# Optimization experiments

Hardware: AMD Instinct MI355X
Metric: run time of the kernel (lower is better)

Reference implementation:

```python
import jax, jax.numpy as jnp
import numpy as np

B, S, DIM, E, K = 8, 8192, 512, 4, 2
EPS = 1e-6


def setup_inputs() -> dict:
    key = jax.random.key(0)
    ks = jax.random.split(key, 4)
    scale = 0.02
    return {
        "x": jax.random.normal(ks[0], (B, S, DIM), dtype=jnp.float32),
        "router_w": jax.random.normal(ks[1], (DIM, E), dtype=jnp.float32) * scale,
        "router_b": jnp.zeros((E,), jnp.float32),
        "expert_w": jax.random.normal(ks[2], (E, DIM, DIM), dtype=jnp.float32) * scale,
        "expert_b": jnp.zeros((E, DIM), jnp.float32),
        "out_w": jax.random.normal(ks[3], (DIM, DIM), dtype=jnp.float32) * scale,
        "out_b": jnp.zeros((DIM,), jnp.float32),
        "norm_w": jnp.ones((DIM,), jnp.float32),
    }


def reference(x, router_w, router_b, expert_w, expert_b, out_w, out_b, norm_w):
    b, s, d = x.shape
    # router
    logits = x @ router_w + router_b                      # [B,S,E]
    topw, topi = jax.lax.top_k(logits, K)                 # [B,S,K]
    topw = jax.nn.softmax(topw, axis=-1)
    t = b * s
    xf = x.reshape(t, d)
    idx = topi.reshape(t, K)
    w = topw.reshape(t, K).astype(x.dtype)
    # dense token-expert weight mask (topk indices are distinct per token)
    mask = jnp.zeros((t, E), x.dtype).at[jnp.arange(t)[:, None], idx].set(w)
    # expert FFN: Linear + SiLU (dropout disabled in eval)
    h = jax.nn.silu(jnp.einsum("td,edh->teh", xf, expert_w) + expert_b)  # [T,E,D]
    comb = jnp.einsum("te,teh->th", mask, h)              # weighted combine
    out = comb @ out_w + out_b
    y = xf + out                                          # residual
    rms = jnp.sqrt(jnp.mean(y * y, axis=-1, keepdims=True) + EPS)
    return (norm_w * (y / rms)).reshape(b, s, d)
```

## Files before the change

kernel.cpp:

```cpp
#include <hip/hip_runtime.h>
#include <hip/hip_bf16.h>
#include <stdint.h>

#define NTOK 65536
#define DIM 512
#define NEXP 4
#define REG 14336

using u16 = unsigned short;
using u32 = unsigned int;
typedef __attribute__((ext_vector_type(4))) float f32x4;
typedef __attribute__((ext_vector_type(8))) short bf16x8;
typedef __attribute__((ext_vector_type(8))) u16 u16x8;
typedef __attribute__((ext_vector_type(4))) u16 u16x4;

__device__ __forceinline__ u16 f2bf(float f) {
  u32 u = __builtin_bit_cast(u32, f);
  u32 r = (u + 0x7FFFu + ((u >> 16) & 1u)) >> 16;
  return (u16)r;
}
__device__ __forceinline__ float bf2f(u16 v) {
  return __builtin_bit_cast(float, (u32)v << 16);
}

#define GLOAD_LDS16(gp, lp)                                                    \
  __builtin_amdgcn_global_load_lds(                                            \
      (const __attribute__((address_space(1))) void*)(gp),                     \
      (__attribute__((address_space(3))) void*)(lp), 16, 0, 0)

#define FENCE asm volatile("" ::: "memory")
#define BARRIER { FENCE; __builtin_amdgcn_s_barrier(); FENCE; }
#define VMCNT_(n) asm volatile("s_waitcnt vmcnt(" #n ")" ::: "memory")
#define VMCNT(n) VMCNT_(n)
#define SB __builtin_amdgcn_sched_barrier(0)

__device__ __forceinline__ const bf16x8* lds_frag(const u16* base, int row, int chunk) {
  return (const bf16x8*)((const char*)base + row * 128 + (((chunk) ^ (row & 7)) << 4));
}

__global__ void packw(const float* __restrict__ ew, const float* __restrict__ ow,
                      u16* __restrict__ ewtp, u16* __restrict__ owt3,
                      int* __restrict__ cnt) {
  if (blockIdx.x == 0 && threadIdx.x < 6) cnt[threadIdx.x] = 0;
  int lane = threadIdx.x & 63, wv = threadIdx.x >> 6;
  int gf = blockIdx.x * 4 + wv;
  int r16 = lane & 15, lg = lane >> 4;
  u16x8 o;
  if (gf < 2048) {
    int hs = gf & 31, T = (gf >> 5) & 15, e = gf >> 9;
    int h = hs * 16 + r16;
    int d0 = T * 32 + lg * 8;
#pragma unroll
    for (int q = 0; q < 8; ++q)
      o[q] = f2bf(ew[((size_t)e * DIM + d0 + q) * DIM + h]);
    *(u16x8*)(ewtp + (size_t)gf * 512 + lane * 8) = o;
  } else {
    int frag = gf - 2048;
    int j = frag & 7, kc = (frag >> 3) & 1, t = (frag >> 4) & 7, strip = frag >> 7;
    int h = strip * 128 + j * 16 + r16;
    int d0 = t * 64 + kc * 32 + lg * 8;
#pragma unroll
    for (int q = 0; q < 8; ++q) o[q] = f2bf(ow[(size_t)(d0 + q) * DIM + h]);
    *(u16x8*)(owt3 + (size_t)frag * 512 + lane * 8) = o;
  }
}

__global__ void router_kernel(const float* __restrict__ x, const float* __restrict__ rw,
                              const float* __restrict__ rb, u16* __restrict__ xb,
                              int* __restrict__ pp, float2* __restrict__ wab) {
  int lane = threadIdx.x & 63, wave = threadIdx.x >> 6;
  size_t t = (size_t)blockIdx.x * 4 + wave;
  const float* xr = x + t * DIM + lane * 8;
  f32x4 v0 = *(const f32x4*)xr;
  f32x4 v1 = *(const f32x4*)(xr + 4);
  float l0 = 0.f, l1 = 0.f, l2 = 0.f, l3 = 0.f;
  const float* rwp = rw + (size_t)lane * 32;
#pragma unroll
  for (int j = 0; j < 8; ++j) {
    float xv = (j < 4) ? v0[j] : v1[j - 4];
    f32x4 r = *(const f32x4*)(rwp + j * 4);
    l0 += xv * r[0]; l1 += xv * r[1]; l2 += xv * r[2]; l3 += xv * r[3];
  }
#pragma unroll
  for (int off = 32; off; off >>= 1) {
    l0 += __shfl_xor(l0, off); l1 += __shfl_xor(l1, off);
    l2 += __shfl_xor(l2, off); l3 += __shfl_xor(l3, off);
  }
  float lv[4] = {l0 + rb[0], l1 + rb[1], l2 + rb[2], l3 + rb[3]};
  int i0 = 0; float b0 = lv[0];
#pragma unroll
  for (int e = 1; e < 4; ++e) if (lv[e] > b0) { b0 = lv[e]; i0 = e; }
  int i1 = (i0 == 0) ? 1 : 0; float b1 = lv[i1];
#pragma unroll
  for (int e = 0; e < 4; ++e) if (e != i0 && lv[e] > b1) { b1 = lv[e]; i1 = e; }
  float ex = __expf(b1 - b0);
  float w0 = 1.0f / (1.0f + ex);
  float w1 = ex * w0;
  if (lane == 0) {
    int a = (i0 < i1) ? i0 : i1;
    int b = (i0 < i1) ? i1 : i0;
    const int ptab[16] = {-1, 0, 1, 2, -1, -1, 3, 4, -1, -1, -1, 5, -1, -1, -1, -1};
    pp[t] = ptab[a * 4 + b];
    float wa = (a == i0) ? w0 : w1;
    float wb = (a == i0) ? w1 : w0;
    wab[t] = make_float2(wa, wb);
  }
  u16x8 o;
#pragma unroll
  for (int j = 0; j < 4; ++j) { o[j] = f2bf(v0[j]); o[4 + j] = f2bf(v1[j]); }
  *(u16x8*)(xb + t * DIM + lane * 8) = o;
}

__global__ void assignscatter(const int* __restrict__ pp, const float2* __restrict__ wab,
                              int* __restrict__ cnt, int* __restrict__ list,
                              float2* __restrict__ wpair) {
  int t = blockIdx.x * 256 + threadIdx.x;
  int lane = threadIdx.x & 63;
  int p = pp[t];
  float2 w = wab[t];
  int pos = 0;
#pragma unroll
  for (int q = 0; q < 6; ++q) {
    unsigned long long m = __ballot(p == q);
    if (p == q) {
      int rank = __popcll(m & ((1ull << lane) - 1ull));
      int leader = __ffsll((long long)m) - 1;
      int base = 0;
      if (lane == leader) base = atomicAdd(&cnt[q], (int)__popcll(m));
      base = __shfl(base, leader);
      pos = base + rank;
    }
  }
  int slot = p * REG + pos;
  if (pos < REG) {
    list[slot] = t;
    wpair[slot] = w;
  }
}

__global__ __launch_bounds__(256, 2) void expert_gemm(
    const u16* __restrict__ xb, const u16* __restrict__ ewtp,
    const float* __restrict__ ebias, const int* __restrict__ cnt,
    const int* __restrict__ list, const float2* __restrict__ wpair,
    u16* __restrict__ comb) {
  __shared__ u16 Asl[3][128 * 64];
  int tid = threadIdx.x, lane = tid & 63, wave = tid >> 6;
  int wy = wave >> 1, wx = wave & 1;
  int b = blockIdx.x;
  int chunk = b >> 5, within = b & 31;
  int panel = chunk * 8 + (within & 7);
  int nblk = within >> 3;
  int p = panel / (REG / 128);
  int m0 = panel * 128;
  int cntp = cnt[p];
  if (m0 - p * REG >= cntp) return;
  int n0 = nblk * 128;
  const int ea2[6] = {0, 0, 0, 1, 1, 2};
  const int eb2[6] = {1, 2, 3, 2, 3, 3};
  int eA = ea2[p], eB = eb2[p];

  int r16 = lane & 15, lg = lane >> 4;
  int rl = lane >> 3;
  int scb = ((lane & 7) ^ rl) * 8;
  int s = r16 & 7;
  int ab0 = (wy * 64 + r16) * 128 + ((s >> 2) << 6) + ((lg ^ (s & 3)) << 4);
  int ab1 = ab0 ^ 64;

  int sid[4];
#pragma unroll
  for (int j = 0; j < 4; ++j) {
    int slot = m0 + wave * 32 + j * 8 + rl;
    int idv = list[slot];
    sid[j] = ((slot - p * REG) < cntp) ? idv : 0;
  }
  const u16* a0b = xb + (size_t)sid[0] * DIM + scb;
  const u16* a1b = xb + (size_t)sid[1] * DIM + scb;
  const u16* a2b = xb + (size_t)sid[2] * DIM + scb;
  const u16* a3b = xb + (size_t)sid[3] * DIM + scb;
  const u16* bpA = ewtp + (size_t)eA * 262144 + (size_t)(n0 / 16 + wx * 4) * 512 + lane * 8;
  const u16* bpB = ewtp + (size_t)eB * 262144 + (size_t)(n0 / 16 + wx * 4) * 512 + lane * 8;

  f32x4 accA[4][4], accB[4][4];
#pragma unroll
  for (int i = 0; i < 4; ++i)
#pragma unroll
    for (int j = 0; j < 4; ++j) { accA[i][j] = (f32x4)(0.f); accB[i][j] = (f32x4)(0.f); }

#define STAGE(BI, KS)                                                          \
  do {                                                                         \
    GLOAD_LDS16(a0b + (KS) * 64, Asl[BI] + (wave * 32) * 64);                  \
    GLOAD_LDS16(a1b + (KS) * 64, Asl[BI] + (wave * 32 + 8) * 64);              \
    GLOAD_LDS16(a2b + (KS) * 64, Asl[BI] + (wave * 32 + 16) * 64);             \
    GLOAD_LDS16(a3b + (KS) * 64, Asl[BI] + (wave * 32 + 24) * 64);             \
  } while (0)
#define LOADB(BV, T32)                                                         \
  do {                                                                         \
    _Pragma("unroll") for (int i = 0; i < 4; ++i) {                            \
      BV[i]     = *(const bf16x8*)(bpA + (T32) * 16384 + i * 512);             \
      BV[4 + i] = *(const bf16x8*)(bpB + (T32) * 16384 + i * 512);             \
    }                                                                          \
  } while (0)

  STAGE(0, 0); SB;
  STAGE(1, 1); SB;
  VMCNT(4);
  BARRIER;

  bf16x8 Bk0[8], Bk1[8];
#define KST(T, WC)                                                             \
  {                                                                            \
    LOADB(Bk0, 2 * (T));                                                       \
    LOADB(Bk1, 2 * (T) + 1);                                                   \
    SB;                                                                        \
    if ((T) + 2 < 8) { STAGE(((T) + 2) % 3, (T) + 2); }                        \
    SB;                                                                        \
    const char* Ab_ = (const char*)Asl[(T) % 3];                               \
    bf16x8 a[4];                                                               \
    _Pragma("unroll") for (int i = 0; i < 4; ++i)                              \
      a[i] = *(const bf16x8*)(Ab_ + ab0 + i * 2048);                           \
    __builtin_amdgcn_s_setprio(1);                                             \
    _Pragma("unroll") for (int i = 0; i < 4; ++i)                              \
      _Pragma("unroll") for (int j = 0; j < 4; ++j)                            \
        accA[i][j] = __builtin_amdgcn_mfma_f32_16x16x32_bf16(a[i], Bk0[j], accA[i][j], 0, 0, 0); \
    _Pragma("unroll") for (int i = 0; i < 4; ++i)                              \
      _Pragma("unroll") for (int j = 0; j < 4; ++j)                            \
        accB[i][j] = __builtin_amdgcn_mfma_f32_16x16x32_bf16(a[i], Bk0[4 + j], accB[i][j], 0, 0, 0); \
    __builtin_amdgcn_s_setprio(0);                                             \
    _Pragma("unroll") for (int i = 0; i < 4; ++i)                              \
      a[i] = *(const bf16x8*)(Ab_ + ab1 + i * 2048);                           \
    __builtin_amdgcn_s_setprio(1);                                             \
    _Pragma("unroll") for (int i = 0; i < 4; ++i)                              \
      _Pragma("unroll") for (int j = 0; j < 4; ++j)                            \
        accA[i][j] = __builtin_amdgcn_mfma_f32_16x16x32_bf16(a[i], Bk1[j], accA[i][j], 0, 0, 0); \
    _Pragma("unroll") for (int i = 0; i < 4; ++i)                              \
      _Pragma("unroll") for (int j = 0; j < 4; ++j)                            \
        accB[i][j] = __builtin_amdgcn_mfma_f32_16x16x32_bf16(a[i], Bk1[4 + j], accB[i][j], 0, 0, 0); \
    __builtin_amdgcn_s_setprio(0);                                             \
    WC;                                                                        \
  }

  KST(0, { VMCNT(4); BARRIER; })
  KST(1, { VMCNT(4); BARRIER; })
  KST(2, { VMCNT(4); BARRIER; })
  KST(3, { VMCNT(4); BARRIER; })
  KST(4, { VMCNT(4); BARRIER; })
  KST(5, { VMCNT(4); BARRIER; })
  KST(6, { VMCNT(0); BARRIER; })
  KST(7, {})
#undef KST
#undef LOADB
#undef STAGE

  float bA4[4], bB4[4];
#pragma unroll
  for (int j = 0; j < 4; ++j) {
    int h = n0 + wx * 64 + j * 16 + r16;
    bA4[j] = ebias[eA * DIM + h];
    bB4[j] = ebias[eB * DIM + h];
  }
#pragma unroll
  for (int i = 0; i < 4; ++i) {
    int rb = wy * 64 + i * 16 + lg * 4;
#pragma unroll
    for (int rr = 0; rr < 4; ++rr) {
      int slot = m0 + rb + rr;
      bool val = (slot - p * REG) < cntp;
      int id = list[slot];
      float2 wv = wpair[slot];
#pragma unroll
      for (int j = 0; j < 4; ++j) {
        float zA = accA[i][j][rr] + bA4[j];
        float zB = accB[i][j][rr] + bB4[j];
        float sA = zA / (1.0f + __expf(-zA));
        float sB = zB / (1.0f + __expf(-zB));
        float v = wv.x * sA + wv.y * sB;
        if (val) {
          int h = n0 + wx * 64 + j * 16 + r16;
          comb[(size_t)id * DIM + h] = f2bf(v);
        }
      }
    }
  }
}

__global__ __launch_bounds__(256, 2) void outnorm(
    const u16* __restrict__ comb, const u16* __restrict__ owt3,
    const float* __restrict__ ob, const u16* __restrict__ xb,
    const float* __restrict__ nw, float* __restrict__ out) {
  __shared__ u16 As[3][64 * 64];
  __shared__ float rowsum[64][4];
  int tid = threadIdx.x, lane = tid & 63, w = tid >> 6;
  int m0 = blockIdx.x * 64;
  int r16 = lane & 15, lg = lane >> 4;
  int rl = lane >> 3;
  int scb = ((lane & 7) ^ rl) * 8;
  int n0w = w * 128;

  f32x4 acc[8][4];
#pragma unroll
  for (int j = 0; j < 8; ++j)
#pragma unroll
    for (int i = 0; i < 4; ++i) acc[j][i] = (f32x4)(0.f);

#define OSTG(bi, ks)                                                           \
  _Pragma("unroll") for (int jj = 0; jj < 2; ++jj) {                           \
    GLOAD_LDS16(comb + (size_t)(m0 + w * 16 + jj * 8 + rl) * DIM + (ks) * 64 + scb, \
                As[bi] + (w * 16 + jj * 8) * 64);                              \
  }
#define LOADB(BV, HH)                                                          \
  {                                                                            \
    const u16* bp_ = owt3 +                                                    \
        ((size_t)(((w * 8 + ((HH) >> 1)) * 2 + ((HH) & 1)) * 8)) * 512 + lane * 8; \
    _Pragma("unroll") for (int jj = 0; jj < 8; ++jj)                           \
      BV[jj] = *(const bf16x8*)(bp_ + jj * 512);                               \
  }
#define HSTEP(H, BC, BN, WC)                                                   \
  {                                                                            \
    if (((H) & 1) == 0 && ((H) >> 1) + 2 < 8) OSTG((((H) >> 1) + 2) % 3, ((H) >> 1) + 2); \
    if ((H) + 1 < 16) LOADB(BN, (H) + 1);                                      \
    bf16x8 af[4];                                                              \
    _Pragma("unroll") for (int ii = 0; ii < 4; ++ii)                           \
      af[ii] = *lds_frag(As[((H) >> 1) % 3], ii * 16 + r16, ((H) & 1) * 4 + lg); \
    __builtin_amdgcn_s_setprio(1);                                             \
    _Pragma("unroll") for (int jj = 0; jj < 8; ++jj)                           \
      _Pragma("unroll") for (int ii = 0; ii < 4; ++ii)                         \
        acc[jj][ii] = __builtin_amdgcn_mfma_f32_16x16x32_bf16(BC[jj], af[ii], acc[jj][ii], 0, 0, 0); \
    __builtin_amdgcn_s_setprio(0);                                             \
    WC;                                                                        \
  }

  bf16x8 BE[8], BO[8];
  OSTG(0, 0); OSTG(1, 1);
  LOADB(BE, 0);
  VMCNT(10);
  BARRIER;

  HSTEP(0,  BE, BO, {})
  HSTEP(1,  BO, BE, { VMCNT(10); BARRIER; })
  HSTEP(2,  BE, BO, {})
  HSTEP(3,  BO, BE, { VMCNT(10); BARRIER; })
  HSTEP(4,  BE, BO, {})
  HSTEP(5,  BO, BE, { VMCNT(10); BARRIER; })
  HSTEP(6,  BE, BO, {})
  HSTEP(7,  BO, BE, { VMCNT(10); BARRIER; })
  HSTEP(8,  BE, BO, {})
  HSTEP(9,  BO, BE, { VMCNT(10); BARRIER; })
  HSTEP(10, BE, BO, {})
  HSTEP(11, BO, BE, { VMCNT(10); BARRIER; })
  HSTEP(12, BE, BO, {})
  HSTEP(13, BO, BE, { VMCNT(8); BARRIER; })
  HSTEP(14, BE, BO, {})
  HSTEP(15, BO, BE, {})
#undef HSTEP
#undef LOADB
#undef OSTG

  float part[4] = {0.f, 0.f, 0.f, 0.f};
#pragma unroll
  for (int hj = 0; hj < 8; ++hj) {
    int h0 = n0w + hj * 16 + lg * 4;
    f32x4 obv = *(const f32x4*)(ob + h0);
#pragma unroll
    for (int ti = 0; ti < 4; ++ti) {
      int t = m0 + ti * 16 + r16;
      u16x4 xv4 = *(const u16x4*)(xb + (size_t)t * DIM + h0);
#pragma unroll
      for (int rr = 0; rr < 4; ++rr) {
        float yv = bf2f(xv4[rr]) + acc[hj][ti][rr] + obv[rr];
        acc[hj][ti][rr] = yv;
        part[ti] += yv * yv;
      }
    }
  }
#pragma unroll
  for (int ti = 0; ti < 4; ++ti) {
    part[ti] += __shfl_xor(part[ti], 16);
    part[ti] += __shfl_xor(part[ti], 32);
  }
  if (lane < 16) {
#pragma unroll
    for (int ti = 0; ti < 4; ++ti) rowsum[ti * 16 + r16][w] = part[ti];
  }
  __syncthreads();
  float inv[4];
#pragma unroll
  for (int ti = 0; ti < 4; ++ti) {
    int tr = ti * 16 + r16;
    float s = rowsum[tr][0] + rowsum[tr][1] + rowsum[tr][2] + rowsum[tr][3];
    inv[ti] = 1.0f / sqrtf(s * (1.0f / 512.0f) + 1e-6f);
  }
#pragma unroll
  for (int hj = 0; hj < 8; ++hj) {
    int h0 = n0w + hj * 16 + lg * 4;
    f32x4 nwv = *(const f32x4*)(nw + h0);
#pragma unroll
    for (int ti = 0; ti < 4; ++ti) {
      int t = m0 + ti * 16 + r16;
      f32x4 o;
#pragma unroll
      for (int rr = 0; rr < 4; ++rr) o[rr] = acc[hj][ti][rr] * inv[ti] * nwv[rr];
      *(f32x4*)(out + (size_t)t * DIM + h0) = o;
    }
  }
}

extern "C" void kernel_launch(void* const* d_in, const int* in_sizes, int n_in,
                              void* d_out, int out_size, void* d_ws, size_t ws_size,
                              hipStream_t stream) {
  const float* x  = (const float*)d_in[0];
  const float* rw = (const float*)d_in[1];
  const float* rb = (const float*)d_in[2];
  const float* ew = (const float*)d_in[3];
  const float* eb = (const float*)d_in[4];
  const float* ow = (const float*)d_in[5];
  const float* ob = (const float*)d_in[6];
  const float* nw = (const float*)d_in[7];
  float* out = (float*)d_out;

  char* ws = (char*)d_ws;
  u16*   xb    = (u16*)(ws);
  u16*   combb = (u16*)(ws + 67108864);
  int*   pp    = (int*)(ws + 67108864);
  float2* wab  = (float2*)(ws + 67108864 + 262144);
  u16*   ewtp  = (u16*)(ws + 134217728);
  u16*   owt3  = (u16*)(ws + 136314880);
  int*   list  = (int*)(ws + 136839168);
  float2* wpair = (float2*)(ws + 136839168 + 344064);
  int*   cnt   = (int*)(ws + 136839168 + 344064 + 688128);

  packw<<<640, 256, 0, stream>>>(ew, ow, ewtp, owt3, cnt);
  router_kernel<<<NTOK / 4, 256, 0, stream>>>(x, rw, rb, xb, pp, wab);
  assignscatter<<<NTOK / 256, 256, 0, stream>>>(pp, wab, cnt, list, wpair);
  expert_gemm<<<dim3(6 * REG / 128 * 4), 256, 0, stream>>>(xb, ewtp, eb, cnt, list, wpair, combb);
  outnorm<<<dim3(NTOK / 64), 256, 0, stream>>>(combb, owt3, ob, xb, nw, out);
}
```

Baseline: 317.7 us.

## Halve outnorm row tile to 32 and drop B-fragment double buffering

The outnorm kernel now processes 32 token rows per block instead of 64, halving accumulators and LDS, and raises the launch-bounds occupancy hint to 3 blocks per CU. The register double-buffered prefetch of the output weight fragments is removed; weights are now loaded inside each step, and the vmcnt waits are adjusted to match. This trades more weight reloads per token and less latency hiding for higher occupancy and twice as many blocks.

Measured after the change: 322.5 us. About the same (+1.5%).

```diff
diff --git a/kernel.cpp b/kernel.cpp
--- a/kernel.cpp
+++ b/kernel.cpp
@@ -283,85 +283,80 @@
   }
 }
 
-__global__ __launch_bounds__(256, 2) void outnorm(
+__global__ __launch_bounds__(256, 3) void outnorm(
     const u16* __restrict__ comb, const u16* __restrict__ owt3,
     const float* __restrict__ ob, const u16* __restrict__ xb,
     const float* __restrict__ nw, float* __restrict__ out) {
-  __shared__ u16 As[3][64 * 64];
-  __shared__ float rowsum[64][4];
+  __shared__ u16 As[3][32 * 64];
+  __shared__ float rowsum[32][4];
   int tid = threadIdx.x, lane = tid & 63, w = tid >> 6;
-  int m0 = blockIdx.x * 64;
+  int m0 = blockIdx.x * 32;
   int r16 = lane & 15, lg = lane >> 4;
   int rl = lane >> 3;
   int scb = ((lane & 7) ^ rl) * 8;
   int n0w = w * 128;
 
-  f32x4 acc[8][4];
+  f32x4 acc[8][2];
 #pragma unroll
   for (int j = 0; j < 8; ++j)
 #pragma unroll
-    for (int i = 0; i < 4; ++i) acc[j][i] = (f32x4)(0.f);
+    for (int i = 0; i < 2; ++i) acc[j][i] = (f32x4)(0.f);
 
 #define OSTG(bi, ks)                                                           \
-  _Pragma("unroll") for (int jj = 0; jj < 2; ++jj) {                           \
-    GLOAD_LDS16(comb + (size_t)(m0 + w * 16 + jj * 8 + rl) * DIM + (ks) * 64 + scb, \
-                As[bi] + (w * 16 + jj * 8) * 64);                              \
-  }
-#define LOADB(BV, HH)                                                          \
-  {                                                                            \
-    const u16* bp_ = owt3 +                                                    \
-        ((size_t)(((w * 8 + ((HH) >> 1)) * 2 + ((HH) & 1)) * 8)) * 512 + lane * 8; \
-    _Pragma("unroll") for (int jj = 0; jj < 8; ++jj)                           \
-      BV[jj] = *(const bf16x8*)(bp_ + jj * 512);                               \
-  }
-#define HSTEP(H, BC, BN, WC)                                                   \
+  GLOAD_LDS16(comb + (size_t)(m0 + w * 8 + rl) * DIM + (ks) * 64 + scb,        \
+              As[bi] + (w * 8) * 64)
+
+#define HSTEP(H, WC)                                                           \
   {                                                                            \
     if (((H) & 1) == 0 && ((H) >> 1) + 2 < 8) OSTG((((H) >> 1) + 2) % 3, ((H) >> 1) + 2); \
-    if ((H) + 1 < 16) LOADB(BN, (H) + 1);                                      \
-    bf16x8 af[4];                                                              \
-    _Pragma("unroll") for (int ii = 0; ii < 4; ++ii)                           \
+    bf16x8 bw[8];                                                              \
+    {                                                                          \
+      const u16* bp_ = owt3 +                                                  \
+          ((size_t)(((w * 8 + ((H) >> 1)) * 2 + ((H) & 1)) * 8)) * 512 + lane * 8; \
+      _Pragma("unroll") for (int jj = 0; jj < 8; ++jj)                         \
+        bw[jj] = *(const bf16x8*)(bp_ + jj * 512);                             \
+    }                                                                          \
+    bf16x8 af[2];                                                              \
+    _Pragma("unroll") for (int ii = 0; ii < 2; ++ii)                           \
       af[ii] = *lds_frag(As[((H) >> 1) % 3], ii * 16 + r16, ((H) & 1) * 4 + lg); \
     __builtin_amdgcn_s_setprio(1);                                             \
     _Pragma("unroll") for (int jj = 0; jj < 8; ++jj)                           \
-      _Pragma("unroll") for (int ii = 0; ii < 4; ++ii)                         \
-        acc[jj][ii] = __builtin_amdgcn_mfma_f32_16x16x32_bf16(BC[jj], af[ii], acc[jj][ii], 0, 0, 0); \
+      _Pragma("unroll") for (int ii = 0; ii < 2; ++ii)                         \
+        acc[jj][ii] = __builtin_amdgcn_mfma_f32_16x16x32_bf16(bw[jj], af[ii], acc[jj][ii], 0, 0, 0); \
     __builtin_amdgcn_s_setprio(0);                                             \
     WC;                                                                        \
   }
 
-  bf16x8 BE[8], BO[8];
   OSTG(0, 0); OSTG(1, 1);
-  LOADB(BE, 0);
-  VMCNT(10);
+  VMCNT(1);
   BARRIER;
 
-  HSTEP(0,  BE, BO, {})
-  HSTEP(1,  BO, BE, { VMCNT(10); BARRIER; })
-  HSTEP(2,  BE, BO, {})
-  HSTEP(3,  BO, BE, { VMCNT(10); BARRIER; })
-  HSTEP(4,  BE, BO, {})
-  HSTEP(5,  BO, BE, { VMCNT(10); BARRIER; })
-  HSTEP(6,  BE, BO, {})
-  HSTEP(7,  BO, BE, { VMCNT(10); BARRIER; })
-  HSTEP(8,  BE, BO, {})
-  HSTEP(9,  BO, BE, { VMCNT(10); BARRIER; })
-  HSTEP(10, BE, BO, {})
-  HSTEP(11, BO, BE, { VMCNT(10); BARRIER; })
-  HSTEP(12, BE, BO, {})
-  HSTEP(13, BO, BE, { VMCNT(8); BARRIER; })
-  HSTEP(14, BE, BO, {})
-  HSTEP(15, BO, BE, {})
+  HSTEP(0,  {})
+  HSTEP(1,  { VMCNT(1); BARRIER; })
+  HSTEP(2,  {})
+  HSTEP(3,  { VMCNT(1); BARRIER; })
+  HSTEP(4,  {})
+  HSTEP(5,  { VMCNT(1); BARRIER; })
+  HSTEP(6,  {})
+  HSTEP(7,  { VMCNT(1); BARRIER; })
+  HSTEP(8,  {})
+  HSTEP(9,  { VMCNT(1); BARRIER; })
+  HSTEP(10, {})
+  HSTEP(11, { VMCNT(1); BARRIER; })
+  HSTEP(12, {})
+  HSTEP(13, { VMCNT(0); BARRIER; })
+  HSTEP(14, {})
+  HSTEP(15, {})
 #undef HSTEP
-#undef LOADB
 #undef OSTG
 
-  float part[4] = {0.f, 0.f, 0.f, 0.f};
+  float part[2] = {0.f, 0.f};
 #pragma unroll
   for (int hj = 0; hj < 8; ++hj) {
     int h0 = n0w + hj * 16 + lg * 4;
     f32x4 obv = *(const f32x4*)(ob + h0);
 #pragma unroll
-    for (int ti = 0; ti < 4; ++ti) {
+    for (int ti = 0; ti < 2; ++ti) {
       int t = m0 + ti * 16 + r16;
       u16x4 xv4 = *(const u16x4*)(xb + (size_t)t * DIM + h0);
 #pragma unroll
@@ -373,18 +368,18 @@
     }
   }
 #pragma unroll
-  for (int ti = 0; ti < 4; ++ti) {
+  for (int ti = 0; ti < 2; ++ti) {
     part[ti] += __shfl_xor(part[ti], 16);
     part[ti] += __shfl_xor(part[ti], 32);
   }
   if (lane < 16) {
 #pragma unroll
-    for (int ti = 0; ti < 4; ++ti) rowsum[ti * 16 + r16][w] = part[ti];
+    for (int ti = 0; ti < 2; ++ti) rowsum[ti * 16 + r16][w] = part[ti];
   }
   __syncthreads();
-  float inv[4];
-#pragma unroll
-  for (int ti = 0; ti < 4; ++ti) {
+  float inv[2];
+#pragma unroll
+  for (int ti = 0; ti < 2; ++ti) {
     int tr = ti * 16 + r16;
     float s = rowsum[tr][0] + rowsum[tr][1] + rowsum[tr][2] + rowsum[tr][3];
     inv[ti] = 1.0f / sqrtf(s * (1.0f / 512.0f) + 1e-6f);
@@ -394,7 +389,7 @@
     int h0 = n0w + hj * 16 + lg * 4;
     f32x4 nwv = *(const f32x4*)(nw + h0);
 #pragma unroll
-    for (int ti = 0; ti < 4; ++ti) {
+    for (int ti = 0; ti < 2; ++ti) {
       int t = m0 + ti * 16 + r16;
       f32x4 o;
 #pragma unroll
@@ -432,5 +427,5 @@
   router_kernel<<<NTOK / 4, 256, 0, stream>>>(x, rw, rb, xb, pp, wab);
   assignscatter<<<NTOK / 256, 256, 0, stream>>>(pp, wab, cnt, list, wpair);
   expert_gemm<<<dim3(6 * REG / 128 * 4), 256, 0, stream>>>(xb, ewtp, eb, cnt, list, wpair, combb);
-  outnorm<<<dim3(NTOK / 64), 256, 0, stream>>>(combb, owt3, ob, xb, nw, out);
-}
+  outnorm<<<dim3(NTOK / 32), 256, 0, stream>>>(combb, owt3, ob, xb, nw, out);
+}
```

## Split expert GEMM waves by expert and combine pair outputs through LDS

Applied to the files above, without the earlier changes.

Each block now covers 64 output columns instead of 128. The four waves are split so that two compute expert A and two compute expert B, where before each wave held accumulators for both experts. This halves accumulator and B-register use per wave, which allows launch bounds of 3 blocks per CU, and doubles the grid. The two experts' weighted SiLU results are combined through an LDS exchange with extra barriers. The cost is that the A tile is gathered twice as often per output column.

New measurement: 340.7 us. +7.3%, slower.

```diff
diff --git a/kernel.cpp b/kernel.cpp
--- a/kernel.cpp
+++ b/kernel.cpp
@@ -138,26 +138,27 @@
   }
 }
 
-__global__ __launch_bounds__(256, 2) void expert_gemm(
+__global__ __launch_bounds__(256, 3) void expert_gemm(
     const u16* __restrict__ xb, const u16* __restrict__ ewtp,
     const float* __restrict__ ebias, const int* __restrict__ cnt,
     const int* __restrict__ list, const float2* __restrict__ wpair,
     u16* __restrict__ comb) {
   __shared__ u16 Asl[3][128 * 64];
   int tid = threadIdx.x, lane = tid & 63, wave = tid >> 6;
-  int wy = wave >> 1, wx = wave & 1;
+  int wy = wave & 1;
+  int we = wave >> 1;
   int b = blockIdx.x;
-  int chunk = b >> 5, within = b & 31;
+  int chunk = b >> 6, within = b & 63;
   int panel = chunk * 8 + (within & 7);
   int nblk = within >> 3;
   int p = panel / (REG / 128);
   int m0 = panel * 128;
   int cntp = cnt[p];
   if (m0 - p * REG >= cntp) return;
-  int n0 = nblk * 128;
+  int n0 = nblk * 64;
   const int ea2[6] = {0, 0, 0, 1, 1, 2};
   const int eb2[6] = {1, 2, 3, 2, 3, 3};
-  int eA = ea2[p], eB = eb2[p];
+  int e = we ? eb2[p] : ea2[p];
 
   int r16 = lane & 15, lg = lane >> 4;
   int rl = lane >> 3;
@@ -177,14 +178,13 @@
   const u16* a1b = xb + (size_t)sid[1] * DIM + scb;
   const u16* a2b = xb + (size_t)sid[2] * DIM + scb;
   const u16* a3b = xb + (size_t)sid[3] * DIM + scb;
-  const u16* bpA = ewtp + (size_t)eA * 262144 + (size_t)(n0 / 16 + wx * 4) * 512 + lane * 8;
-  const u16* bpB = ewtp + (size_t)eB * 262144 + (size_t)(n0 / 16 + wx * 4) * 512 + lane * 8;
-
-  f32x4 accA[4][4], accB[4][4];
+  const u16* bp = ewtp + (size_t)e * 262144 + (size_t)(n0 / 16) * 512 + lane * 8;
+
+  f32x4 acc[4][4];
 #pragma unroll
   for (int i = 0; i < 4; ++i)
 #pragma unroll
-    for (int j = 0; j < 4; ++j) { accA[i][j] = (f32x4)(0.f); accB[i][j] = (f32x4)(0.f); }
+    for (int j = 0; j < 4; ++j) acc[i][j] = (f32x4)(0.f);
 
 #define STAGE(BI, KS)                                                          \
   do {                                                                         \
@@ -195,10 +195,8 @@
   } while (0)
 #define LOADB(BV, T32)                                                         \
   do {                                                                         \
-    _Pragma("unroll") for (int i = 0; i < 4; ++i) {                            \
-      BV[i]     = *(const bf16x8*)(bpA + (T32) * 16384 + i * 512);             \
-      BV[4 + i] = *(const bf16x8*)(bpB + (T32) * 16384 + i * 512);             \
-    }                                                                          \
+    _Pragma("unroll") for (int i = 0; i < 4; ++i)                              \
+      BV[i] = *(const bf16x8*)(bp + (T32) * 16384 + i * 512);                  \
   } while (0)
 
   STAGE(0, 0); SB;
@@ -206,7 +204,7 @@
   VMCNT(4);
   BARRIER;
 
-  bf16x8 Bk0[8], Bk1[8];
+  bf16x8 Bk0[4], Bk1[4];
 #define KST(T, WC)                                                             \
   {                                                                            \
     LOADB(Bk0, 2 * (T));                                                       \
@@ -221,20 +219,14 @@
     __builtin_amdgcn_s_setprio(1);                                             \
     _Pragma("unroll") for (int i = 0; i < 4; ++i)                              \
       _Pragma("unroll") for (int j = 0; j < 4; ++j)                            \
-        accA[i][j] = __builtin_amdgcn_mfma_f32_16x16x32_bf16(a[i], Bk0[j], accA[i][j], 0, 0, 0); \
-    _Pragma("unroll") for (int i = 0; i < 4; ++i)                              \
-      _Pragma("unroll") for (int j = 0; j < 4; ++j)                            \
-        accB[i][j] = __builtin_amdgcn_mfma_f32_16x16x32_bf16(a[i], Bk0[4 + j], accB[i][j], 0, 0, 0); \
+        acc[i][j] = __builtin_amdgcn_mfma_f32_16x16x32_bf16(a[i], Bk0[j], acc[i][j], 0, 0, 0); \
     __builtin_amdgcn_s_setprio(0);                                             \
     _Pragma("unroll") for (int i = 0; i < 4; ++i)                              \
       a[i] = *(const bf16x8*)(Ab_ + ab1 + i * 2048);                           \
     __builtin_amdgcn_s_setprio(1);                                             \
     _Pragma("unroll") for (int i = 0; i < 4; ++i)                              \
       _Pragma("unroll") for (int j = 0; j < 4; ++j)                            \
-        accA[i][j] = __builtin_amdgcn_mfma_f32_16x16x32_bf16(a[i], Bk1[j], accA[i][j], 0, 0, 0); \
-    _Pragma("unroll") for (int i = 0; i < 4; ++i)                              \
-      _Pragma("unroll") for (int j = 0; j < 4; ++j)                            \
-        accB[i][j] = __builtin_amdgcn_mfma_f32_16x16x32_bf16(a[i], Bk1[4 + j], accB[i][j], 0, 0, 0); \
+        acc[i][j] = __builtin_amdgcn_mfma_f32_16x16x32_bf16(a[i], Bk1[j], acc[i][j], 0, 0, 0); \
     __builtin_amdgcn_s_setprio(0);                                             \
     WC;                                                                        \
   }
@@ -251,32 +243,55 @@
 #undef LOADB
 #undef STAGE
 
-  float bA4[4], bB4[4];
-#pragma unroll
-  for (int j = 0; j < 4; ++j) {
-    int h = n0 + wx * 64 + j * 16 + r16;
-    bA4[j] = ebias[eA * DIM + h];
-    bB4[j] = ebias[eB * DIM + h];
-  }
-#pragma unroll
-  for (int i = 0; i < 4; ++i) {
-    int rb = wy * 64 + i * 16 + lg * 4;
-#pragma unroll
-    for (int rr = 0; rr < 4; ++rr) {
-      int slot = m0 + rb + rr;
-      bool val = (slot - p * REG) < cntp;
-      int id = list[slot];
-      float2 wv = wpair[slot];
+  float b4[4];
+#pragma unroll
+  for (int j = 0; j < 4; ++j) b4[j] = ebias[e * DIM + n0 + j * 16 + r16];
+  float* ex = (float*)Asl;
+  __syncthreads();
+  if (we == 0) {
+#pragma unroll
+    for (int i = 0; i < 4; ++i) {
+      int tok0 = wy * 64 + i * 16 + lg * 4;
+      float wvx[4];
+#pragma unroll
+      for (int rr = 0; rr < 4; ++rr) wvx[rr] = wpair[m0 + tok0 + rr].x;
 #pragma unroll
       for (int j = 0; j < 4; ++j) {
-        float zA = accA[i][j][rr] + bA4[j];
-        float zB = accB[i][j][rr] + bB4[j];
-        float sA = zA / (1.0f + __expf(-zA));
-        float sB = zB / (1.0f + __expf(-zB));
-        float v = wv.x * sA + wv.y * sB;
-        if (val) {
-          int h = n0 + wx * 64 + j * 16 + r16;
-          comb[(size_t)id * DIM + h] = f2bf(v);
+        f32x4 t;
+#pragma unroll
+        for (int rr = 0; rr < 4; ++rr) {
+          float z = acc[i][j][rr] + b4[j];
+          t[rr] = wvx[rr] * (z / (1.0f + __expf(-z)));
+        }
+        int byte = (j * 16 + r16) * 512 + ((tok0 * 4) ^ ((r16 & 7) << 4));
+        *(f32x4*)((char*)ex + byte) = t;
+      }
+    }
+  }
+  __syncthreads();
+  if (we == 1) {
+#pragma unroll
+    for (int i = 0; i < 4; ++i) {
+      int tok0 = wy * 64 + i * 16 + lg * 4;
+      float wvy[4];
+      int id4[4]; bool val4[4];
+#pragma unroll
+      for (int rr = 0; rr < 4; ++rr) {
+        int slot = m0 + tok0 + rr;
+        wvy[rr] = wpair[slot].y;
+        val4[rr] = (slot - p * REG) < cntp;
+        id4[rr] = list[slot];
+      }
+#pragma unroll
+      for (int j = 0; j < 4; ++j) {
+        int byte = (j * 16 + r16) * 512 + ((tok0 * 4) ^ ((r16 & 7) << 4));
+        f32x4 tv = *(const f32x4*)((const char*)ex + byte);
+        int h = n0 + j * 16 + r16;
+#pragma unroll
+        for (int rr = 0; rr < 4; ++rr) {
+          float z = acc[i][j][rr] + b4[j];
+          float v = tv[rr] + wvy[rr] * (z / (1.0f + __expf(-z)));
+          if (val4[rr]) comb[(size_t)id4[rr] * DIM + h] = f2bf(v);
         }
       }
     }
@@ -431,6 +446,6 @@
   packw<<<640, 256, 0, stream>>>(ew, ow, ewtp, owt3, cnt);
   router_kernel<<<NTOK / 4, 256, 0, stream>>>(x, rw, rb, xb, pp, wab);
   assignscatter<<<NTOK / 256, 256, 0, stream>>>(pp, wab, cnt, list, wpair);
-  expert_gemm<<<dim3(6 * REG / 128 * 4), 256, 0, stream>>>(xb, ewtp, eb, cnt, list, wpair, combb);
+  expert_gemm<<<dim3(6 * REG / 128 * 8), 256, 0, stream>>>(xb, ewtp, eb, cnt, list, wpair, combb);
   outnorm<<<dim3(NTOK / 64), 256, 0, stream>>>(combb, owt3, ob, xb, nw, out);
 }
```
